# Kernel optimization log

Measured on AMD Instinct MI355X. Metric: run time of the kernel, lower is better.

The kernel has to match this reference:

```python
import jax, jax.numpy as jnp
import numpy as np

B, C, N, M, K = 8, 64, 8192, 2048, 16
FPS_RATIO, TAU = 0.7, 0.2


def setup_inputs() -> dict:
    key = jax.random.key(0)
    k1, k2 = jax.random.split(key)
    x = jax.random.normal(k1, (B, C, N), dtype=jnp.float32)
    pos = jax.random.normal(k2, (B, 3, N), dtype=jnp.float32)
    return {"x": x, "pos": pos, "m": M}


def _fps(pts, key, fps_m):
    # pts: [N, 3] -> farthest point sampling indices [fps_m]
    n = pts.shape[0]
    start = jax.random.randint(key, (), 0, n)
    d0 = jnp.full((n,), 1e10, dtype=jnp.float32)

    def step(carry, _):
        dist, last = carry
        d = jnp.sum((pts - pts[last]) ** 2, axis=1)  # [N]
        dist = jnp.minimum(dist, d)
        far = jnp.argmax(dist)
        return (dist, far), far

    (_, _), cents = jax.lax.scan(step, (d0, start), None, length=fps_m - 1)
    return jnp.concatenate([start[None], cents])


def _hybrid_idx(pos, m, fps_ratio, key):
    # pos: [B, 3, N] -> idx [B, m]  (FPS for fps_m points, random for the rest)
    b, _, n = pos.shape
    fps_m = max(1, int(m * fps_ratio))
    rand_m = m - fps_m
    pts = jnp.transpose(pos, (0, 2, 1))  # [B, N, 3]
    keys = jax.random.split(key, b)
    cents = jax.vmap(lambda p, k: _fps(p, k, fps_m))(pts, keys)  # [B, fps_m]
    if rand_m > 0:
        rkeys = jax.random.split(jax.random.fold_in(key, 1), b)
        rand = jax.vmap(lambda k: jax.random.permutation(k, n)[:rand_m])(rkeys)
        idx = jnp.concatenate([cents, rand], axis=1)
    else:
        idx = cents
    return idx[:, :m]


def _gather_neighbor(feat, idx):
    # feat: [B, C, N], idx: [B, m, k] -> [B, C, m, k]
    return jax.vmap(lambda f, i: f[:, i])(feat, idx)


def reference(x, pos, m):
    b = x.shape[0]
    idx = _hybrid_idx(pos, m, FPS_RATIO, jax.random.key(42))  # [B, m]
    pos_sub = jax.vmap(lambda p, i: p[:, i])(pos, idx)  # [B, 3, m]

    # KNN via squared distances (same ordering as euclidean cdist), no grad path
    ps = jax.lax.stop_gradient(jnp.transpose(pos_sub, (0, 2, 1)))  # [B, m, 3]
    pa = jax.lax.stop_gradient(jnp.transpose(pos, (0, 2, 1)))      # [B, N, 3]
    d2 = (jnp.sum(ps * ps, axis=-1)[:, :, None]
          + jnp.sum(pa * pa, axis=-1)[:, None, :]
          - 2.0 * jnp.einsum('bmd,bnd->bmn', ps, pa))  # [B, m, N]
    _, knn_idx = jax.lax.top_k(-d2, K)  # [B, m, K] smallest distances

    neigh_x = _gather_neighbor(x, knn_idx)      # [B, C, m, K]
    neigh_pos = _gather_neighbor(pos, knn_idx)  # [B, 3, m, K]

    d = jnp.linalg.norm(neigh_pos - pos_sub[..., None], axis=1)  # [B, m, K]
    d = jnp.maximum(d, 1e-6)
    w = jax.nn.softmax(-d / max(1e-6, TAU), axis=-1)  # [B, m, K]
    x_sub = jnp.sum(neigh_x * w[:, None, :, :], axis=-1)  # [B, C, m]
    return x_sub, pos_sub
```

## Files before the change

### kernel.cpp

```cpp
#include <hip/hip_runtime.h>

constexpr int NB   = 8;
constexpr int NC   = 64;
constexpr int NN   = 8192;
constexpr int NM   = 2048;
constexpr int NK   = 16;
constexpr int NFPS = 1433;
constexpr int NRAND = NM - NFPS;

constexpr size_t OFF_IDX   = 256;
constexpr size_t OFF_V1    = 66048;
constexpr size_t OFF_XT    = 1377280;

typedef float v2f __attribute__((ext_vector_type(2)));

struct TF { unsigned a, b; };

__device__ __forceinline__ TF tf2(unsigned k0, unsigned k1, unsigned c0, unsigned c1) {
  unsigned ks2 = k0 ^ k1 ^ 0x1BD11BDAu;
  unsigned x0 = c0 + k0;
  unsigned x1 = c1 + k1;
#define TF_R(r) { x0 += x1; x1 = (x1 << r) | (x1 >> (32 - r)); x1 ^= x0; }
  TF_R(13) TF_R(15) TF_R(26) TF_R(6)
  x0 += k1;  x1 += ks2 + 1u;
  TF_R(17) TF_R(29) TF_R(16) TF_R(24)
  x0 += ks2; x1 += k0 + 2u;
  TF_R(13) TF_R(15) TF_R(26) TF_R(6)
  x0 += k0;  x1 += k1 + 3u;
  TF_R(17) TF_R(29) TF_R(16) TF_R(24)
  x0 += k1;  x1 += ks2 + 4u;
  TF_R(13) TF_R(15) TF_R(26) TF_R(6)
  x0 += ks2; x1 += k0 + 5u;
#undef TF_R
  TF r; r.a = x0; r.b = x1; return r;
}

__device__ __forceinline__ float wave_max_dpp(float v) {
  int vi;
  vi = __builtin_amdgcn_update_dpp(__float_as_int(v), __float_as_int(v), 0x111, 0xf, 0xf, false);
  v = fmaxf(v, __int_as_float(vi));
  vi = __builtin_amdgcn_update_dpp(__float_as_int(v), __float_as_int(v), 0x112, 0xf, 0xf, false);
  v = fmaxf(v, __int_as_float(vi));
  vi = __builtin_amdgcn_update_dpp(__float_as_int(v), __float_as_int(v), 0x114, 0xf, 0xf, false);
  v = fmaxf(v, __int_as_float(vi));
  vi = __builtin_amdgcn_update_dpp(__float_as_int(v), __float_as_int(v), 0x118, 0xf, 0xf, false);
  v = fmaxf(v, __int_as_float(vi));
  vi = __builtin_amdgcn_update_dpp(__float_as_int(v), __float_as_int(v), 0x142, 0xa, 0xf, false);
  v = fmaxf(v, __int_as_float(vi));
  vi = __builtin_amdgcn_update_dpp(__float_as_int(v), __float_as_int(v), 0x143, 0xc, 0xf, false);
  v = fmaxf(v, __int_as_float(vi));
  return __int_as_float(__builtin_amdgcn_readlane(__float_as_int(v), 63));
}

constexpr int FPS_BLKS = NB;
constexpr int PERM_BLKS = 2 * NB;
constexpr int TR_BLKS = (NN / 32) * (NC / 32) * NB;

__device__ void bitonic8192_256(unsigned long long* s, int tid) {
  for (unsigned k = 2; k <= 8192u; k <<= 1) {
    for (unsigned j = k >> 1; j > 0; j >>= 1) {
      __syncthreads();
      for (unsigned t = (unsigned)tid; t < 4096u; t += 256u) {
        unsigned i = ((t & ~(j - 1u)) << 1) | (t & (j - 1u));
        unsigned p = i | j;
        bool up = ((i & k) == 0u);
        unsigned long long a = s[i], c = s[p];
        if ((a > c) == up) { s[i] = c; s[p] = a; }
      }
    }
  }
  __syncthreads();
}

__global__ __launch_bounds__(256, 1) void fused1_kernel(const float* __restrict__ pos,
                                                        const float* __restrict__ x,
                                                        int* __restrict__ idx,
                                                        unsigned* __restrict__ v1buf,
                                                        float* __restrict__ xT) {
  __shared__ __align__(16) char smem[98432];
  const int bid = blockIdx.x;
  const int tid = threadIdx.x;

  if (bid < FPS_BLKS) {
    float* ldsX = (float*)smem;
    float* ldsY = (float*)(smem + 32768);
    float* ldsZ = (float*)(smem + 65536);
    float2 (*slot)[4] = (float2(*)[4])(smem + 98304);
    const int b = bid;
    const int wv = tid >> 6, lane = tid & 63;
    const float* pb = pos + (size_t)b * 3 * NN;
    v2f px[16], py[16], pz[16], dist[16];
    const int base = tid * 32;
    const float4* fx = (const float4*)(pb + base);
    const float4* fy = (const float4*)(pb + NN + base);
    const float4* fz = (const float4*)(pb + 2 * NN + base);
#pragma unroll
    for (int q = 0; q < 8; ++q) {
      float4 a = fx[q], c = fy[q], e = fz[q];
      px[2*q].x = a.x; px[2*q].y = a.y; px[2*q+1].x = a.z; px[2*q+1].y = a.w;
      py[2*q].x = c.x; py[2*q].y = c.y; py[2*q+1].x = c.z; py[2*q+1].y = c.w;
      pz[2*q].x = e.x; pz[2*q].y = e.y; pz[2*q+1].x = e.z; pz[2*q+1].y = e.w;
      ((float4*)(ldsX + base))[q] = a;
      ((float4*)(ldsY + base))[q] = c;
      ((float4*)(ldsZ + base))[q] = e;
    }
#pragma unroll
    for (int p = 0; p < 16; ++p) { dist[p].x = 1e10f; dist[p].y = 1e10f; }
    TF kb_ = tf2(0u, 42u, 0u, (unsigned)b);
    TF k2 = tf2(kb_.a, kb_.b, 0u, 1u);
    TF bt = tf2(k2.a, k2.b, 0u, 0u);
    int widx = (int)((bt.a ^ bt.b) & (unsigned)(NN - 1));
    if (tid == 0) idx[b * NM] = widx;
    __syncthreads();
    float cx = ldsX[widx], cy = ldsY[widx], cz = ldsZ[widx];
    for (int it = 1; it < NFPS; ++it) {
      const int par = it & 1;
      float bestv = -1.0f; int bestS = 0;
      {
        v2f cx2; cx2.x = cx; cx2.y = cx;
        v2f cy2; cy2.x = cy; cy2.y = cy;
        v2f cz2; cz2.x = cz; cz2.y = cz;
#pragma unroll
        for (int p = 0; p < 16; ++p) {
#pragma clang fp contract(off)
          v2f dx = px[p] - cx2;
          v2f dy = py[p] - cy2;
          v2f dz = pz[p] - cz2;
          v2f d2 = (dx * dx + dy * dy) + dz * dz;
          float nd0 = fminf(dist[p].x, d2.x);
          float nd1 = fminf(dist[p].y, d2.y);
          dist[p].x = nd0; dist[p].y = nd1;
          bool c0 = nd0 > bestv;
          bestv = c0 ? nd0 : bestv;
          bestS = c0 ? 2*p : bestS;
          bool c1 = nd1 > bestv;
          bestv = c1 ? nd1 : bestv;
          bestS = c1 ? 2*p + 1 : bestS;
        }
      }
      const int gidx = base + bestS;
      const float wm = wave_max_dpp(bestv);
      unsigned long long msk = __ballot(bestv == wm);
      const int fl = (int)__builtin_ctzll(msk);
      const int widxw = __builtin_amdgcn_readlane(gidx, fl);
      if (lane == 0) slot[par][wv] = make_float2(wm, __int_as_float(widxw));
      __syncthreads();
      float2 s0 = slot[par][0], s1 = slot[par][1], s2 = slot[par][2], s3 = slot[par][3];
      if (s1.x > s0.x) s0 = s1;
      if (s3.x > s2.x) s2 = s3;
      if (s2.x > s0.x) s0 = s2;
      widx = __float_as_int(s0.y);
      cx = ldsX[widx]; cy = ldsY[widx]; cz = ldsZ[widx];
      if (tid == 0) idx[b * NM + it] = widx;
    }
  } else if (bid < FPS_BLKS + PERM_BLKS) {
    unsigned long long* s = (unsigned long long*)smem;
    const int pbl = bid - FPS_BLKS;
    const int b = pbl >> 1, r = pbl & 1;
    TF keyr = tf2(0u, 42u, 0u, 1u);
    TF rk = tf2(keyr.a, keyr.b, 0u, (unsigned)b);
    TF s1k = tf2(rk.a, rk.b, 0u, 1u);
    TF nk  = tf2(rk.a, rk.b, 0u, 0u);
    TF s2k = tf2(nk.a, nk.b, 0u, 1u);
    const unsigned ka = r ? s2k.a : s1k.a;
    const unsigned kb = r ? s2k.b : s1k.b;
    for (int i = tid; i < NN; i += 256) {
      TF t = tf2(ka, kb, 0u, (unsigned)i);
      s[i] = ((unsigned long long)(t.a ^ t.b) << 32) | (unsigned)i;
    }
    bitonic8192_256(s, tid);
    if (r == 0) {
      unsigned* v1 = v1buf + (size_t)b * NN;
      for (int i = tid; i < NN; i += 256) v1[i] = (unsigned)(s[i] & 0xffffffffu);
    } else {
      for (int t = tid; t < NRAND; t += 256)
        idx[b * NM + NFPS + t] = (int)(s[t] & 0xffffffffu);
    }
  } else {
    float (*t)[33] = (float(*)[33])smem;
    const int tt = bid - (FPS_BLKS + PERM_BLKS);
    const int n0 = (tt & 255) * 32;
    const int c0 = ((tt >> 8) & 1) * 32;
    const int b = tt >> 9;
    const int tx = tid & 31, ty0 = tid >> 5;
#pragma unroll
    for (int r = 0; r < 4; ++r) {
      const int ty = ty0 + r * 8;
      t[ty][tx] = x[((size_t)b * NC + (c0 + ty)) * NN + n0 + tx];
    }
    __syncthreads();
#pragma unroll
    for (int r = 0; r < 4; ++r) {
      const int ty = ty0 + r * 8;
      xT[((size_t)b * NN + (n0 + ty)) * NC + c0 + tx] = t[tx][ty];
    }
  }
}

constexpr int KNN_BLKS = NB * NM / 4;
constexpr int POSSUB_BLKS = (NB * 3 * NM + 255) / 256;

__global__ __launch_bounds__(256) void fused3_kernel(const float* __restrict__ pos,
                                                     const int* __restrict__ idx,
                                                     const unsigned* __restrict__ v1,
                                                     const float* __restrict__ xT,
                                                     float* __restrict__ xOut,
                                                     float* __restrict__ posOut) {
  __shared__ unsigned long long lst[4][NK][64];
  __shared__ float tile[64][4];
  const int tid = threadIdx.x;
  if (blockIdx.x >= KNN_BLKS) {
    int i = (blockIdx.x - KNN_BLKS) * 256 + tid;
    if (i < NB * 3 * NM) {
      int mm = i & (NM - 1);
      int bd = i >> 11;
      int d = bd % 3, b = bd / 3;
      int raw = idx[b * NM + mm];
      int id = (mm < NFPS) ? raw : (int)v1[(size_t)b * NN + raw];
      posOut[i] = pos[((size_t)b * 3 + d) * NN + id];
    }
    return;
  }
  const int wv = tid >> 6, lane = tid & 63;
  const int g = blockIdx.x * 4 + wv;
  const int b = g >> 11, mm = g & (NM - 1);
  const float* pb = pos + (size_t)b * 3 * NN;
  const int raw = idx[b * NM + mm];
  const int id = (mm < NFPS) ? raw : (int)v1[(size_t)b * NN + raw];
  const float sx = pb[id], sy = pb[NN + id], sz = pb[2 * NN + id];
  const float sm = __fadd_rn(__fadd_rn(__fmul_rn(sx, sx), __fmul_rn(sy, sy)),
                             __fmul_rn(sz, sz));
  float key[NK]; int kid[NK];
#pragma unroll
  for (int i = 0; i < NK; ++i) { key[i] = __int_as_float(0x7F800000); kid[i] = 0; }
  for (int t = 0; t < NN / 256; ++t) {
    const int n0 = t * 256 + lane * 4;
    const float4 xv = *(const float4*)(pb + n0);
    const float4 yv = *(const float4*)(pb + NN + n0);
    const float4 zv = *(const float4*)(pb + 2 * NN + n0);
#pragma unroll
    for (int j = 0; j < 4; ++j) {
      const float x = (j == 0) ? xv.x : (j == 1) ? xv.y : (j == 2) ? xv.z : xv.w;
      const float y = (j == 0) ? yv.x : (j == 1) ? yv.y : (j == 2) ? yv.z : yv.w;
      const float z = (j == 0) ? zv.x : (j == 1) ? zv.y : (j == 2) ? zv.z : zv.w;
      float sn = __fadd_rn(__fadd_rn(__fmul_rn(x, x), __fmul_rn(y, y)), __fmul_rn(z, z));
      float dt = __fadd_rn(__fadd_rn(__fmul_rn(sx, x), __fmul_rn(sy, y)), __fmul_rn(sz, z));
      float d2 = __fsub_rn(__fadd_rn(sm, sn), __fmul_rn(2.0f, dt));
      const float ck = d2; const int ci = n0 + j;
#pragma unroll
      for (int i = NK - 1; i >= 1; --i) {
        float lo = key[i-1], hi = key[i];
        bool cLo = ck < lo, cHi = ck < hi;
        key[i] = __builtin_amdgcn_fmed3f(ck, lo, hi);
        kid[i] = cLo ? kid[i-1] : (cHi ? ci : kid[i]);
      }
      bool c0 = ck < key[0];
      kid[0] = c0 ? ci : kid[0];
      key[0] = fminf(key[0], ck);
    }
  }
#pragma unroll
  for (int i = 0; i < NK; ++i) {
    unsigned u = __float_as_uint(key[i]);
    u = (u & 0x80000000u) ? ~u : (u | 0x80000000u);
    lst[wv][i][lane] = ((unsigned long long)u << 32) | (unsigned)kid[i];
  }
  int ptr = 0;
  unsigned long long head = lst[wv][0][lane];
  unsigned myn = 0;
  for (int k = 0; k < NK; ++k) {
    unsigned long long mn = head;
#pragma unroll
    for (int off = 32; off > 0; off >>= 1) {
      unsigned long long o = __shfl_xor(mn, off, 64);
      if (o < mn) mn = o;
    }
    if (head == mn) { ++ptr; head = (ptr < NK) ? lst[wv][ptr][lane] : ~0ull; }
    if (lane == k) myn = (unsigned)(mn & 0xffffffffu);
  }
  const int kk = lane & 15;
  const int nk = (int)__shfl(myn, kk, 64);
  float dx = __fsub_rn(pb[nk], sx);
  float dy = __fsub_rn(pb[NN + nk], sy);
  float dz = __fsub_rn(pb[2 * NN + nk], sz);
  float dd = __fadd_rn(__fadd_rn(__fmul_rn(dx, dx), __fmul_rn(dy, dy)),
                       __fmul_rn(dz, dz));
  float d = __fsqrt_rn(dd);
  d = fmaxf(d, 1e-6f);
  float e = __fdiv_rn(0.0f - d, 0.2f);
  float mx = e;
#pragma unroll
  for (int off = 8; off > 0; off >>= 1) mx = fmaxf(mx, __shfl_xor(mx, off, 16));
  float ex = expf(__fsub_rn(e, mx));
  float sum = ex;
#pragma unroll
  for (int off = 8; off > 0; off >>= 1) sum = __fadd_rn(sum, __shfl_xor(sum, off, 16));
  float wgt = __fdiv_rn(ex, sum);
  float acc = 0.0f;
#pragma unroll
  for (int k = 0; k < NK; ++k) {
    float wk = __shfl(wgt, k, 64);
    int   nn = __shfl(nk, k, 64);
    acc = __fadd_rn(acc, __fmul_rn(wk, xT[((size_t)b * NN + nn) * NC + lane]));
  }
  tile[lane][wv] = acc;
  __syncthreads();
  const int m0 = (blockIdx.x * 4) & (NM - 1);
  {
    int c = tid >> 2, ml = tid & 3;
    xOut[((size_t)b * NC + c) * NM + m0 + ml] = tile[c][ml];
  }
}

extern "C" void kernel_launch(void* const* d_in, const int* in_sizes, int n_in,
                              void* d_out, int out_size, void* d_ws, size_t ws_size,
                              hipStream_t stream) {
  const float* x   = (const float*)d_in[0];
  const float* pos = (const float*)d_in[1];
  float* xOut   = (float*)d_out;
  float* posOut = xOut + (size_t)NB * NC * NM;

  char* w = (char*)d_ws;
  int*      idx    = (int*)(w + OFF_IDX);
  unsigned* v1     = (unsigned*)(w + OFF_V1);
  float*    xT     = (float*)(w + OFF_XT);

  hipLaunchKernelGGL(fused1_kernel, dim3(FPS_BLKS + PERM_BLKS + TR_BLKS), dim3(256), 0,
                     stream, pos, x, idx, v1, xT);
  hipLaunchKernelGGL(fused3_kernel, dim3(KNN_BLKS + POSSUB_BLKS), dim3(256), 0, stream,
                     pos, idx, v1, xT, xOut, posOut);
}
```

Measured before the change: 1.561 ms.

## Merge stages into persistent cooperative kernel with flag-based fine-grained dependencies

Replaces the two-kernel pipeline with one persistent kernel. Eight blocks run FPS and publish each index atomically, while worker blocks transpose x, meet at a grid barrier, run the permutation sort, then process KNN groups by spinning on per-entry ready flags. The aim is to overlap KNN and gather work with the serial FPS loop instead of waiting for the whole first kernel. The risks are spin-waiting blocks, reduced parallelism for KNN on only 248 blocks, memset overhead, and possible deadlock if not all blocks are co-resident in the non-cooperative fallback.

```diff
diff --git a/kernel.cpp b/kernel.cpp
--- a/kernel.cpp
+++ b/kernel.cpp
@@ -8,6 +8,7 @@
 constexpr int NFPS = 1433;
 constexpr int NRAND = NM - NFPS;
 
+constexpr size_t OFF_CTR   = 0;
 constexpr size_t OFF_IDX   = 256;
 constexpr size_t OFF_V1    = 66048;
 constexpr size_t OFF_XT    = 1377280;
@@ -52,31 +53,36 @@
   return __int_as_float(__builtin_amdgcn_readlane(__float_as_int(v), 63));
 }
 
+__device__ __forceinline__ int spin_load_i(const int* p) {
+  int v = __hip_atomic_load(p, __ATOMIC_RELAXED, __HIP_MEMORY_SCOPE_AGENT);
+  while (v == -1) {
+    __builtin_amdgcn_s_sleep(2);
+    v = __hip_atomic_load(p, __ATOMIC_RELAXED, __HIP_MEMORY_SCOPE_AGENT);
+  }
+  return v;
+}
+__device__ __forceinline__ unsigned spin_load_u(const unsigned* p) {
+  unsigned v = __hip_atomic_load(p, __ATOMIC_RELAXED, __HIP_MEMORY_SCOPE_AGENT);
+  while (v == 0xFFFFFFFFu) {
+    __builtin_amdgcn_s_sleep(2);
+    v = __hip_atomic_load(p, __ATOMIC_RELAXED, __HIP_MEMORY_SCOPE_AGENT);
+  }
+  return v;
+}
+
 constexpr int FPS_BLKS = NB;
-constexpr int PERM_BLKS = 2 * NB;
-constexpr int TR_BLKS = (NN / 32) * (NC / 32) * NB;
-
-__device__ void bitonic8192_256(unsigned long long* s, int tid) {
-  for (unsigned k = 2; k <= 8192u; k <<= 1) {
-    for (unsigned j = k >> 1; j > 0; j >>= 1) {
-      __syncthreads();
-      for (unsigned t = (unsigned)tid; t < 4096u; t += 256u) {
-        unsigned i = ((t & ~(j - 1u)) << 1) | (t & (j - 1u));
-        unsigned p = i | j;
-        bool up = ((i & k) == 0u);
-        unsigned long long a = s[i], c = s[p];
-        if ((a > c) == up) { s[i] = c; s[p] = a; }
-      }
-    }
-  }
-  __syncthreads();
-}
-
-__global__ __launch_bounds__(256, 1) void fused1_kernel(const float* __restrict__ pos,
-                                                        const float* __restrict__ x,
-                                                        int* __restrict__ idx,
-                                                        unsigned* __restrict__ v1buf,
-                                                        float* __restrict__ xT) {
+constexpr int NW = 256 - FPS_BLKS;
+constexpr int TR_TILES = (NN / 32) * (NC / 32) * NB;
+constexpr int KNN_GRPS = NB * NM / 4;
+
+__global__ __launch_bounds__(256, 1) void mega_kernel(const float* __restrict__ pos,
+                                                      const float* __restrict__ x,
+                                                      int* __restrict__ idx,
+                                                      unsigned* __restrict__ v1buf,
+                                                      float* __restrict__ xT,
+                                                      float* __restrict__ xOut,
+                                                      float* __restrict__ posOut,
+                                                      unsigned* __restrict__ ctr) {
   __shared__ __align__(16) char smem[98432];
   const int bid = blockIdx.x;
   const int tid = threadIdx.x;
@@ -110,7 +116,8 @@
     TF k2 = tf2(kb_.a, kb_.b, 0u, 1u);
     TF bt = tf2(k2.a, k2.b, 0u, 0u);
     int widx = (int)((bt.a ^ bt.b) & (unsigned)(NN - 1));
-    if (tid == 0) idx[b * NM] = widx;
+    if (tid == 0)
+      __hip_atomic_store(&idx[b * NM], widx, __ATOMIC_RELAXED, __HIP_MEMORY_SCOPE_AGENT);
     __syncthreads();
     float cx = ldsX[widx], cy = ldsY[widx], cz = ldsZ[widx];
     for (int it = 1; it < NFPS; ++it) {
@@ -151,12 +158,48 @@
       if (s2.x > s0.x) s0 = s2;
       widx = __float_as_int(s0.y);
       cx = ldsX[widx]; cy = ldsY[widx]; cz = ldsZ[widx];
-      if (tid == 0) idx[b * NM + it] = widx;
-    }
-  } else if (bid < FPS_BLKS + PERM_BLKS) {
+      if (tid == 0)
+        __hip_atomic_store(&idx[b * NM + it], widx, __ATOMIC_RELAXED, __HIP_MEMORY_SCOPE_AGENT);
+    }
+    return;
+  }
+
+  const int w = bid - FPS_BLKS;
+
+  {
+    float (*t)[33] = (float(*)[33])smem;
+    const int tx = tid & 31, ty0 = tid >> 5;
+    for (int tt = w; tt < TR_TILES; tt += NW) {
+      const int n0 = (tt & 255) * 32;
+      const int c0 = ((tt >> 8) & 1) * 32;
+      const int bb = tt >> 9;
+#pragma unroll
+      for (int r = 0; r < 4; ++r) {
+        const int ty = ty0 + r * 8;
+        t[ty][tx] = x[((size_t)bb * NC + (c0 + ty)) * NN + n0 + tx];
+      }
+      __syncthreads();
+#pragma unroll
+      for (int r = 0; r < 4; ++r) {
+        const int ty = ty0 + r * 8;
+        xT[((size_t)bb * NN + (n0 + ty)) * NC + c0 + tx] = t[tx][ty];
+      }
+      __syncthreads();
+    }
+  }
+  __threadfence();
+  __syncthreads();
+  if (tid == 0) {
+    atomicAdd(ctr, 1u);
+    while (__hip_atomic_load(ctr, __ATOMIC_RELAXED, __HIP_MEMORY_SCOPE_AGENT) < (unsigned)NW)
+      __builtin_amdgcn_s_sleep(8);
+  }
+  __syncthreads();
+  __threadfence();
+
+  if (w < 16) {
     unsigned long long* s = (unsigned long long*)smem;
-    const int pbl = bid - FPS_BLKS;
-    const int b = pbl >> 1, r = pbl & 1;
+    const int b = w >> 1, r = w & 1;
     TF keyr = tf2(0u, 42u, 0u, 1u);
     TF rk = tf2(keyr.a, keyr.b, 0u, (unsigned)b);
     TF s1k = tf2(rk.a, rk.b, 0u, 1u);
@@ -168,147 +211,137 @@
       TF t = tf2(ka, kb, 0u, (unsigned)i);
       s[i] = ((unsigned long long)(t.a ^ t.b) << 32) | (unsigned)i;
     }
-    bitonic8192_256(s, tid);
+    for (unsigned k = 2; k <= 8192u; k <<= 1) {
+      for (unsigned j = k >> 1; j > 0; j >>= 1) {
+        __syncthreads();
+        for (unsigned t2 = (unsigned)tid; t2 < 4096u; t2 += 256u) {
+          unsigned i = ((t2 & ~(j - 1u)) << 1) | (t2 & (j - 1u));
+          unsigned p = i | j;
+          bool up = ((i & k) == 0u);
+          unsigned long long a = s[i], c = s[p];
+          if ((a > c) == up) { s[i] = c; s[p] = a; }
+        }
+      }
+    }
+    __syncthreads();
     if (r == 0) {
       unsigned* v1 = v1buf + (size_t)b * NN;
-      for (int i = tid; i < NN; i += 256) v1[i] = (unsigned)(s[i] & 0xffffffffu);
+      for (int i = tid; i < NN; i += 256)
+        __hip_atomic_store(&v1[i], (unsigned)(s[i] & 0xffffffffu),
+                           __ATOMIC_RELAXED, __HIP_MEMORY_SCOPE_AGENT);
     } else {
-      for (int t = tid; t < NRAND; t += 256)
-        idx[b * NM + NFPS + t] = (int)(s[t] & 0xffffffffu);
-    }
-  } else {
-    float (*t)[33] = (float(*)[33])smem;
-    const int tt = bid - (FPS_BLKS + PERM_BLKS);
-    const int n0 = (tt & 255) * 32;
-    const int c0 = ((tt >> 8) & 1) * 32;
-    const int b = tt >> 9;
-    const int tx = tid & 31, ty0 = tid >> 5;
-#pragma unroll
-    for (int r = 0; r < 4; ++r) {
-      const int ty = ty0 + r * 8;
-      t[ty][tx] = x[((size_t)b * NC + (c0 + ty)) * NN + n0 + tx];
-    }
-    __syncthreads();
-#pragma unroll
-    for (int r = 0; r < 4; ++r) {
-      const int ty = ty0 + r * 8;
-      xT[((size_t)b * NN + (n0 + ty)) * NC + c0 + tx] = t[tx][ty];
-    }
-  }
-}
-
-constexpr int KNN_BLKS = NB * NM / 4;
-constexpr int POSSUB_BLKS = (NB * 3 * NM + 255) / 256;
-
-__global__ __launch_bounds__(256) void fused3_kernel(const float* __restrict__ pos,
-                                                     const int* __restrict__ idx,
-                                                     const unsigned* __restrict__ v1,
-                                                     const float* __restrict__ xT,
-                                                     float* __restrict__ xOut,
-                                                     float* __restrict__ posOut) {
-  __shared__ unsigned long long lst[4][NK][64];
-  __shared__ float tile[64][4];
-  const int tid = threadIdx.x;
-  if (blockIdx.x >= KNN_BLKS) {
-    int i = (blockIdx.x - KNN_BLKS) * 256 + tid;
-    if (i < NB * 3 * NM) {
-      int mm = i & (NM - 1);
-      int bd = i >> 11;
-      int d = bd % 3, b = bd / 3;
-      int raw = idx[b * NM + mm];
-      int id = (mm < NFPS) ? raw : (int)v1[(size_t)b * NN + raw];
-      posOut[i] = pos[((size_t)b * 3 + d) * NN + id];
-    }
-    return;
-  }
-  const int wv = tid >> 6, lane = tid & 63;
-  const int g = blockIdx.x * 4 + wv;
-  const int b = g >> 11, mm = g & (NM - 1);
-  const float* pb = pos + (size_t)b * 3 * NN;
-  const int raw = idx[b * NM + mm];
-  const int id = (mm < NFPS) ? raw : (int)v1[(size_t)b * NN + raw];
-  const float sx = pb[id], sy = pb[NN + id], sz = pb[2 * NN + id];
-  const float sm = __fadd_rn(__fadd_rn(__fmul_rn(sx, sx), __fmul_rn(sy, sy)),
-                             __fmul_rn(sz, sz));
-  float key[NK]; int kid[NK];
-#pragma unroll
-  for (int i = 0; i < NK; ++i) { key[i] = __int_as_float(0x7F800000); kid[i] = 0; }
-  for (int t = 0; t < NN / 256; ++t) {
-    const int n0 = t * 256 + lane * 4;
-    const float4 xv = *(const float4*)(pb + n0);
-    const float4 yv = *(const float4*)(pb + NN + n0);
-    const float4 zv = *(const float4*)(pb + 2 * NN + n0);
-#pragma unroll
-    for (int j = 0; j < 4; ++j) {
-      const float x = (j == 0) ? xv.x : (j == 1) ? xv.y : (j == 2) ? xv.z : xv.w;
-      const float y = (j == 0) ? yv.x : (j == 1) ? yv.y : (j == 2) ? yv.z : yv.w;
-      const float z = (j == 0) ? zv.x : (j == 1) ? zv.y : (j == 2) ? zv.z : zv.w;
-      float sn = __fadd_rn(__fadd_rn(__fmul_rn(x, x), __fmul_rn(y, y)), __fmul_rn(z, z));
-      float dt = __fadd_rn(__fadd_rn(__fmul_rn(sx, x), __fmul_rn(sy, y)), __fmul_rn(sz, z));
-      float d2 = __fsub_rn(__fadd_rn(sm, sn), __fmul_rn(2.0f, dt));
-      const float ck = d2; const int ci = n0 + j;
-#pragma unroll
-      for (int i = NK - 1; i >= 1; --i) {
-        float lo = key[i-1], hi = key[i];
-        bool cLo = ck < lo, cHi = ck < hi;
-        key[i] = __builtin_amdgcn_fmed3f(ck, lo, hi);
-        kid[i] = cLo ? kid[i-1] : (cHi ? ci : kid[i]);
-      }
-      bool c0 = ck < key[0];
-      kid[0] = c0 ? ci : kid[0];
-      key[0] = fminf(key[0], ck);
-    }
-  }
-#pragma unroll
-  for (int i = 0; i < NK; ++i) {
-    unsigned u = __float_as_uint(key[i]);
-    u = (u & 0x80000000u) ? ~u : (u | 0x80000000u);
-    lst[wv][i][lane] = ((unsigned long long)u << 32) | (unsigned)kid[i];
-  }
-  int ptr = 0;
-  unsigned long long head = lst[wv][0][lane];
-  unsigned myn = 0;
-  for (int k = 0; k < NK; ++k) {
-    unsigned long long mn = head;
-#pragma unroll
-    for (int off = 32; off > 0; off >>= 1) {
-      unsigned long long o = __shfl_xor(mn, off, 64);
-      if (o < mn) mn = o;
-    }
-    if (head == mn) { ++ptr; head = (ptr < NK) ? lst[wv][ptr][lane] : ~0ull; }
-    if (lane == k) myn = (unsigned)(mn & 0xffffffffu);
-  }
-  const int kk = lane & 15;
-  const int nk = (int)__shfl(myn, kk, 64);
-  float dx = __fsub_rn(pb[nk], sx);
-  float dy = __fsub_rn(pb[NN + nk], sy);
-  float dz = __fsub_rn(pb[2 * NN + nk], sz);
-  float dd = __fadd_rn(__fadd_rn(__fmul_rn(dx, dx), __fmul_rn(dy, dy)),
-                       __fmul_rn(dz, dz));
-  float d = __fsqrt_rn(dd);
-  d = fmaxf(d, 1e-6f);
-  float e = __fdiv_rn(0.0f - d, 0.2f);
-  float mx = e;
-#pragma unroll
-  for (int off = 8; off > 0; off >>= 1) mx = fmaxf(mx, __shfl_xor(mx, off, 16));
-  float ex = expf(__fsub_rn(e, mx));
-  float sum = ex;
-#pragma unroll
-  for (int off = 8; off > 0; off >>= 1) sum = __fadd_rn(sum, __shfl_xor(sum, off, 16));
-  float wgt = __fdiv_rn(ex, sum);
-  float acc = 0.0f;
-#pragma unroll
-  for (int k = 0; k < NK; ++k) {
-    float wk = __shfl(wgt, k, 64);
-    int   nn = __shfl(nk, k, 64);
-    acc = __fadd_rn(acc, __fmul_rn(wk, xT[((size_t)b * NN + nn) * NC + lane]));
-  }
-  tile[lane][wv] = acc;
+      for (int t2 = tid; t2 < NRAND; t2 += 256)
+        __hip_atomic_store(&idx[b * NM + NFPS + t2], (int)(s[t2] & 0xffffffffu),
+                           __ATOMIC_RELAXED, __HIP_MEMORY_SCOPE_AGENT);
+    }
+  }
   __syncthreads();
-  const int m0 = (blockIdx.x * 4) & (NM - 1);
+
   {
-    int c = tid >> 2, ml = tid & 3;
-    xOut[((size_t)b * NC + c) * NM + m0 + ml] = tile[c][ml];
+    unsigned long long (*lst)[NK][64] = (unsigned long long(*)[NK][64])smem;
+    float (*tile)[4] = (float(*)[4])(smem + 32768);
+    const int wv = tid >> 6, lane = tid & 63;
+    for (int g4 = w; g4 < KNN_GRPS; g4 += NW) {
+      const int g = g4 * 4 + wv;
+      const int b = g >> 11, mm = g & (NM - 1);
+      const float* pb = pos + (size_t)b * 3 * NN;
+      const int raw = spin_load_i(&idx[b * NM + mm]);
+      const int id = (mm < NFPS) ? raw : (int)spin_load_u(&v1buf[(size_t)b * NN + raw]);
+      const float sx = pb[id], sy = pb[NN + id], sz = pb[2 * NN + id];
+      const float sm = __fadd_rn(__fadd_rn(__fmul_rn(sx, sx), __fmul_rn(sy, sy)),
+                                 __fmul_rn(sz, sz));
+      float key[NK]; int kid[NK];
+#pragma unroll
+      for (int i = 0; i < NK; ++i) { key[i] = __int_as_float(0x7F800000); kid[i] = 0; }
+      for (int t = 0; t < NN / 256; ++t) {
+        const int n0 = t * 256 + lane * 4;
+        const float4 xv = *(const float4*)(pb + n0);
+        const float4 yv = *(const float4*)(pb + NN + n0);
+        const float4 zv = *(const float4*)(pb + 2 * NN + n0);
+#pragma unroll
+        for (int j = 0; j < 4; ++j) {
+          const float xx = (j == 0) ? xv.x : (j == 1) ? xv.y : (j == 2) ? xv.z : xv.w;
+          const float yy = (j == 0) ? yv.x : (j == 1) ? yv.y : (j == 2) ? yv.z : yv.w;
+          const float zz = (j == 0) ? zv.x : (j == 1) ? zv.y : (j == 2) ? zv.z : zv.w;
+          float sn = __fadd_rn(__fadd_rn(__fmul_rn(xx, xx), __fmul_rn(yy, yy)), __fmul_rn(zz, zz));
+          float dt = __fadd_rn(__fadd_rn(__fmul_rn(sx, xx), __fmul_rn(sy, yy)), __fmul_rn(sz, zz));
+          float d2 = __fsub_rn(__fadd_rn(sm, sn), __fmul_rn(2.0f, dt));
+          const float ck = d2; const int ci = n0 + j;
+#pragma unroll
+          for (int i = NK - 1; i >= 1; --i) {
+            float lo = key[i-1], hi = key[i];
+            bool cLo = ck < lo, cHi = ck < hi;
+            key[i] = __builtin_amdgcn_fmed3f(ck, lo, hi);
+            kid[i] = cLo ? kid[i-1] : (cHi ? ci : kid[i]);
+          }
+          bool c0 = ck < key[0];
+          kid[0] = c0 ? ci : kid[0];
+          key[0] = fminf(key[0], ck);
+        }
+      }
+#pragma unroll
+      for (int i = 0; i < NK; ++i) {
+        unsigned u = __float_as_uint(key[i]);
+        u = (u & 0x80000000u) ? ~u : (u | 0x80000000u);
+        lst[wv][i][lane] = ((unsigned long long)u << 32) | (unsigned)kid[i];
+      }
+      int ptr = 0;
+      unsigned long long head = lst[wv][0][lane];
+      unsigned myn = 0;
+      for (int k = 0; k < NK; ++k) {
+        unsigned long long mn = head;
+#pragma unroll
+        for (int off = 32; off > 0; off >>= 1) {
+          unsigned long long o = __shfl_xor(mn, off, 64);
+          if (o < mn) mn = o;
+        }
+        if (head == mn) { ++ptr; head = (ptr < NK) ? lst[wv][ptr][lane] : ~0ull; }
+        if (lane == k) myn = (unsigned)(mn & 0xffffffffu);
+      }
+      const int kk = lane & 15;
+      const int nk = (int)__shfl(myn, kk, 64);
+      float dx = __fsub_rn(pb[nk], sx);
+      float dy = __fsub_rn(pb[NN + nk], sy);
+      float dz = __fsub_rn(pb[2 * NN + nk], sz);
+      float dd = __fadd_rn(__fadd_rn(__fmul_rn(dx, dx), __fmul_rn(dy, dy)),
+                           __fmul_rn(dz, dz));
+      float d = __fsqrt_rn(dd);
+      d = fmaxf(d, 1e-6f);
+      float e = __fdiv_rn(0.0f - d, 0.2f);
+      float mx = e;
+#pragma unroll
+      for (int off = 8; off > 0; off >>= 1) mx = fmaxf(mx, __shfl_xor(mx, off, 16));
+      float ex = expf(__fsub_rn(e, mx));
+      float sum = ex;
+#pragma unroll
+      for (int off = 8; off > 0; off >>= 1) sum = __fadd_rn(sum, __shfl_xor(sum, off, 16));
+      float wgt = __fdiv_rn(ex, sum);
+      float acc = 0.0f;
+#pragma unroll
+      for (int k = 0; k < NK; ++k) {
+        float wk = __shfl(wgt, k, 64);
+        int   nn = __shfl(nk, k, 64);
+        acc = __fadd_rn(acc, __fmul_rn(wk, xT[((size_t)b * NN + nn) * NC + lane]));
+      }
+      tile[lane][wv] = acc;
+      __syncthreads();
+      const int m0 = (g4 * 4) & (NM - 1);
+      const int bb = (g4 * 4) >> 11;
+      {
+        int c = tid >> 2, ml = tid & 3;
+        xOut[((size_t)bb * NC + c) * NM + m0 + ml] = tile[c][ml];
+      }
+      __syncthreads();
+    }
+  }
+
+  for (int i = w * 256 + tid; i < NB * 3 * NM; i += NW * 256) {
+    int mm = i & (NM - 1);
+    int bd = i >> 11;
+    int d = bd % 3, b = bd / 3;
+    int raw = spin_load_i(&idx[b * NM + mm]);
+    int id = (mm < NFPS) ? raw : (int)spin_load_u(&v1buf[(size_t)b * NN + raw]);
+    posOut[i] = pos[((size_t)b * 3 + d) * NN + id];
   }
 }
 
@@ -321,12 +354,20 @@
   float* posOut = xOut + (size_t)NB * NC * NM;
 
   char* w = (char*)d_ws;
-  int*      idx    = (int*)(w + OFF_IDX);
-  unsigned* v1     = (unsigned*)(w + OFF_V1);
-  float*    xT     = (float*)(w + OFF_XT);
-
-  hipLaunchKernelGGL(fused1_kernel, dim3(FPS_BLKS + PERM_BLKS + TR_BLKS), dim3(256), 0,
-                     stream, pos, x, idx, v1, xT);
-  hipLaunchKernelGGL(fused3_kernel, dim3(KNN_BLKS + POSSUB_BLKS), dim3(256), 0, stream,
-                     pos, idx, v1, xT, xOut, posOut);
-}
+  unsigned* ctr = (unsigned*)(w + OFF_CTR);
+  int*      idx = (int*)(w + OFF_IDX);
+  unsigned* v1  = (unsigned*)(w + OFF_V1);
+  float*    xT  = (float*)(w + OFF_XT);
+
+  hipMemsetAsync(w + OFF_CTR, 0, 256, stream);
+  hipMemsetAsync(w + OFF_IDX, 0xFF, OFF_V1 - OFF_IDX + (size_t)NB * NN * 4, stream);
+
+  void* args[] = {(void*)&pos, (void*)&x, (void*)&idx, (void*)&v1,
+                  (void*)&xT, (void*)&xOut, (void*)&posOut, (void*)&ctr};
+  hipError_t e = hipLaunchCooperativeKernel((const void*)mega_kernel, dim3(256), dim3(256),
+                                            args, 0, stream);
+  if (e != hipSuccess) {
+    hipLaunchKernelGGL(mega_kernel, dim3(256), dim3(256), 0, stream,
+                       pos, x, idx, v1, xT, xOut, posOut, ctr);
+  }
+}
```

New measurement: 1.967 ms. +26.0%, slower.
